# Kernel optimization log

Hardware: AMD Instinct MI355X
Metric: run time of the kernel (lower is better)

The kernel has to match this reference:

```python
import jax, jax.numpy as jnp
import numpy as np
import math

EMBED_DIM = 512
NUM_HEADS = 8
B, T = 1, 4096

def setup_inputs() -> dict:
    key = jax.random.key(0)
    ks = jax.random.split(key, 12)
    D = EMBED_DIM
    s = 1.0 / math.sqrt(D)
    inp = {
        "x": jax.random.normal(ks[0], (B, T, D), dtype=jnp.float32),
        "ln1_scale": jnp.ones((D,), jnp.float32),
        "ln1_bias": jnp.zeros((D,), jnp.float32),
        "Wq": jax.random.normal(ks[1], (D, D), jnp.float32) * s,
        "bq": jnp.zeros((D,), jnp.float32),
        "Wk": jax.random.normal(ks[2], (D, D), jnp.float32) * s,
        "bk": jnp.zeros((D,), jnp.float32),
        "Wv": jax.random.normal(ks[3], (D, D), jnp.float32) * s,
        "bv": jnp.zeros((D,), jnp.float32),
        "Wo": jax.random.normal(ks[4], (D, D), jnp.float32) * s,
        "bo": jnp.zeros((D,), jnp.float32),
        "ln2_scale": jnp.ones((D,), jnp.float32),
        "ln2_bias": jnp.zeros((D,), jnp.float32),
        "W1": jax.random.normal(ks[5], (D, 4 * D), jnp.float32) * s,
        "b1": jnp.zeros((4 * D,), jnp.float32),
        "W2": jax.random.normal(ks[6], (4 * D, D), jnp.float32) * (1.0 / math.sqrt(4 * D)),
        "b2": jnp.zeros((D,), jnp.float32),
    }
    return inp

def _layernorm(x, scale, bias, eps=1e-6):
    mu = jnp.mean(x, axis=-1, keepdims=True)
    var = jnp.mean(jnp.square(x - mu), axis=-1, keepdims=True)
    return (x - mu) * jax.lax.rsqrt(var + eps) * scale + bias

def reference(x, ln1_scale, ln1_bias, Wq, bq, Wk, bk, Wv, bv, Wo, bo,
              ln2_scale, ln2_bias, W1, b1, W2, b2):
    Bb, Tt, D = x.shape
    H = NUM_HEADS
    hd = D // H
    residual = x
    h = _layernorm(x, ln1_scale, ln1_bias)
    q = (h @ Wq + bq).reshape(Bb, Tt, H, hd).transpose(0, 2, 1, 3)
    k = (h @ Wk + bk).reshape(Bb, Tt, H, hd).transpose(0, 2, 1, 3)
    v = (h @ Wv + bv).reshape(Bb, Tt, H, hd).transpose(0, 2, 1, 3)
    # [B,H,T,T] scores (naive attention as in the original module)
    scores = jnp.einsum('bhqd,bhkd->bhqk', q, k) / math.sqrt(hd)
    probs = jax.nn.softmax(scores, axis=-1)
    out = jnp.einsum('bhqk,bhkd->bhqd', probs, v).transpose(0, 2, 1, 3).reshape(Bb, Tt, D)
    h = out @ Wo + bo  # dropout deterministic -> identity
    x = h + residual
    residual = x
    h = _layernorm(x, ln2_scale, ln2_bias)
    h = jax.nn.gelu(h @ W1 + b1, approximate=True)
    h = h @ W2 + b2
    return h + residual
```

## Files before the change

### kernel.cpp

```cpp
#include <hip/hip_runtime.h>
#include <hip/hip_bf16.h>
#include <stdint.h>

typedef __bf16 bf16;
typedef __bf16 bf16x4 __attribute__((ext_vector_type(4)));
typedef __bf16 bf16x8 __attribute__((ext_vector_type(8)));
typedef float  f32x4  __attribute__((ext_vector_type(4)));
typedef float  f32x16 __attribute__((ext_vector_type(16)));

#define MFMA16(A_, B_, C_) __builtin_amdgcn_mfma_f32_16x16x32_bf16((A_), (B_), (C_), 0, 0, 0)
#define MFMA32(A_, B_, C_) __builtin_amdgcn_mfma_f32_32x32x16_bf16((A_), (B_), (C_), 0, 0, 0)

#define QSCALE 0.1803368801111137f

__device__ __forceinline__ void gload_lds16(const void* g, void* l) {
  __builtin_amdgcn_global_load_lds(
      (const __attribute__((address_space(1))) unsigned int*)g,
      (__attribute__((address_space(3))) unsigned int*)l, 16, 0, 0);
}

__device__ __forceinline__ unsigned pk2(float lo, float hi_) {
  union { bf16 h[2]; unsigned u; } t;
  t.h[0] = (bf16)lo; t.h[1] = (bf16)hi_;
  return t.u;
}

__global__ __launch_bounds__(256) void prep(const float* __restrict__ Wq,
                                            const float* __restrict__ Wk,
                                            const float* __restrict__ Wv,
                                            const float* __restrict__ Wo,
                                            const float* __restrict__ W1,
                                            const float* __restrict__ W2,
                                            const float* __restrict__ bq,
                                            const float* __restrict__ bk,
                                            const float* __restrict__ bv,
                                            bf16* __restrict__ wqkvT, bf16* __restrict__ woT,
                                            bf16* __restrict__ w1T, bf16* __restrict__ w2T,
                                            float* __restrict__ bqkv) {
  const int b = blockIdx.x;
  if (b >= 768) {
    int i = (b - 768) * 256 + threadIdx.x;
    if (i < 1536)
      bqkv[i] = (i < 512) ? bq[i] * QSCALE : (i < 1024 ? bk[i - 512] : bv[i - 1024]);
    return;
  }
  const float* in; bf16* outp; int K, N, t; float sc = 1.f;
  if (b < 64)       { in = Wq; outp = wqkvT;              K = 512;  N = 512;  t = b;       sc = QSCALE; }
  else if (b < 128) { in = Wk; outp = wqkvT + 512 * 512;  K = 512;  N = 512;  t = b - 64;  }
  else if (b < 192) { in = Wv; outp = wqkvT + 1024 * 512; K = 512;  N = 512;  t = b - 128; }
  else if (b < 256) { in = Wo; outp = woT;                K = 512;  N = 512;  t = b - 192; }
  else if (b < 512) { in = W1; outp = w1T;                K = 512;  N = 2048; t = b - 256; }
  else              { in = W2; outp = w2T;                K = 2048; N = 512;  t = b - 512; }
  const int tx = K >> 6;
  const int k0 = (t % tx) * 64, n0 = (t / tx) * 64;
  __shared__ bf16 tile[64][72];
  const int tid = threadIdx.x;
#pragma unroll
  for (int s = 0; s < 16; ++s) {
    int j = tid + s * 256;
    int r = j >> 6, c = j & 63;
    tile[r][c] = (bf16)(in[(size_t)(k0 + r) * N + n0 + c] * sc);
  }
  __syncthreads();
#pragma unroll
  for (int s = 0; s < 16; ++s) {
    int j = tid + s * 256;
    int n = j >> 6, k = j & 63;
    outp[(size_t)(n0 + n) * K + k0 + k] = tile[k][n];
  }
}

__global__ __launch_bounds__(256) void ln_k(const float* __restrict__ x,
                                            const float* __restrict__ sc,
                                            const float* __restrict__ bi,
                                            bf16* __restrict__ out) {
  const int w = threadIdx.x >> 6, l = threadIdx.x & 63;
  const int row = blockIdx.x * 4 + w;
  const float4* xp = (const float4*)(x + (size_t)row * 512 + l * 8);
  float4 v0 = xp[0], v1 = xp[1];
  float xv[8] = {v0.x, v0.y, v0.z, v0.w, v1.x, v1.y, v1.z, v1.w};
  float s = 0.f, q = 0.f;
#pragma unroll
  for (int j = 0; j < 8; ++j) { s += xv[j]; q += xv[j] * xv[j]; }
#pragma unroll
  for (int m = 1; m < 64; m <<= 1) { s += __shfl_xor(s, m); q += __shfl_xor(q, m); }
  const float mean = s * (1.f / 512.f);
  const float var = q * (1.f / 512.f) - mean * mean;
  const float rstd = rsqrtf(var + 1e-6f);
  const float4* scp = (const float4*)(sc + l * 8);
  const float4* bip = (const float4*)(bi + l * 8);
  float4 s0 = scp[0], s1 = scp[1], b0 = bip[0], b1 = bip[1];
  float sv[8] = {s0.x, s0.y, s0.z, s0.w, s1.x, s1.y, s1.z, s1.w};
  float bv[8] = {b0.x, b0.y, b0.z, b0.w, b1.x, b1.y, b1.z, b1.w};
  bf16x8 ov;
#pragma unroll
  for (int j = 0; j < 8; ++j) ov[j] = (bf16)((xv[j] - mean) * rstd * sv[j] + bv[j]);
  *(bf16x8*)(out + (size_t)row * 512 + l * 8) = ov;
}

__global__ __launch_bounds__(256) void ln2_comb(const float* __restrict__ p0,
                                                const float* __restrict__ p1,
                                                const float* __restrict__ x,
                                                const float* __restrict__ bo,
                                                const float* __restrict__ sc,
                                                const float* __restrict__ bi,
                                                float* __restrict__ x2,
                                                bf16* __restrict__ h2) {
  const int w = threadIdx.x >> 6, l = threadIdx.x & 63;
  const int row = blockIdx.x * 4 + w;
  const size_t base = (size_t)row * 512 + l * 8;
  float xv[8];
#pragma unroll
  for (int j = 0; j < 2; ++j) {
    float4 a = *(const float4*)(p0 + base + j * 4);
    float4 b = *(const float4*)(p1 + base + j * 4);
    float4 c = *(const float4*)(x + base + j * 4);
    float4 d = *(const float4*)(bo + l * 8 + j * 4);
    xv[j * 4 + 0] = a.x + b.x + c.x + d.x;
    xv[j * 4 + 1] = a.y + b.y + c.y + d.y;
    xv[j * 4 + 2] = a.z + b.z + c.z + d.z;
    xv[j * 4 + 3] = a.w + b.w + c.w + d.w;
  }
  *(float4*)(x2 + base) = make_float4(xv[0], xv[1], xv[2], xv[3]);
  *(float4*)(x2 + base + 4) = make_float4(xv[4], xv[5], xv[6], xv[7]);
  float s = 0.f, q = 0.f;
#pragma unroll
  for (int j = 0; j < 8; ++j) { s += xv[j]; q += xv[j] * xv[j]; }
#pragma unroll
  for (int m = 1; m < 64; m <<= 1) { s += __shfl_xor(s, m); q += __shfl_xor(q, m); }
  const float mean = s * (1.f / 512.f);
  const float var = q * (1.f / 512.f) - mean * mean;
  const float rstd = rsqrtf(var + 1e-6f);
  const float4* scp = (const float4*)(sc + l * 8);
  const float4* bip = (const float4*)(bi + l * 8);
  float4 s0 = scp[0], s1 = scp[1], b0 = bip[0], b1 = bip[1];
  float sv[8] = {s0.x, s0.y, s0.z, s0.w, s1.x, s1.y, s1.z, s1.w};
  float bv[8] = {b0.x, b0.y, b0.z, b0.w, b1.x, b1.y, b1.z, b1.w};
  bf16x8 ov;
#pragma unroll
  for (int j = 0; j < 8; ++j) ov[j] = (bf16)((xv[j] - mean) * rstd * sv[j] + bv[j]);
  *(bf16x8*)(h2 + base) = ov;
}

__global__ __launch_bounds__(256) void final_comb(const float* __restrict__ parts, int nsplit,
                                                  const float* __restrict__ b2,
                                                  const float* __restrict__ x2,
                                                  float* __restrict__ outp) {
  const int i4 = blockIdx.x * 256 + threadIdx.x;
  const size_t off = (size_t)i4 * 4;
  float4 acc = *(const float4*)(x2 + off);
  float4 bb = *(const float4*)(b2 + (off & 511));
  acc.x += bb.x; acc.y += bb.y; acc.z += bb.z; acc.w += bb.w;
  for (int z = 0; z < nsplit; ++z) {
    float4 p = *(const float4*)(parts + (size_t)z * 4096 * 512 + off);
    acc.x += p.x; acc.y += p.y; acc.z += p.z; acc.w += p.w;
  }
  *(float4*)(outp + off) = acc;
}

template <int EPI>
__global__ __launch_bounds__(256) void gemm_bt(const bf16* __restrict__ A,
                                               const bf16* __restrict__ Bt,
                                               const float* __restrict__ bias,
                                               const float* __restrict__ res,
                                               void* __restrict__ outp,
                                               int M, int N, int K) {
  __shared__ bf16 a_lds[128 * 64];
  __shared__ bf16 b_lds[128 * 64];
  const int m0 = blockIdx.x * 128, n0 = blockIdx.y * 128;
  const int tid = threadIdx.x, l = tid & 63, w = tid >> 6;
  const int wm = w >> 1, wn = w & 1;
  const int lc = l & 15, g = l >> 4;
  const int srow = l >> 3;
  const int cs = (l & 7) ^ srow;

  f32x4 acc[4][4] = {};
  const int kiters = K >> 6;
  for (int kt = 0; kt < kiters; ++kt) {
    const int k0 = kt << 6;
#pragma unroll
    for (int r = 0; r < 4; ++r) {
      const int rg = r * 32 + w * 8;
      gload_lds16(A + (size_t)(m0 + rg + srow) * K + k0 + cs * 8,
                  (char*)a_lds + rg * 128);
      gload_lds16(Bt + (size_t)(n0 + rg + srow) * K + k0 + cs * 8,
                  (char*)b_lds + rg * 128);
    }
    __syncthreads();
#pragma unroll
    for (int kk = 0; kk < 2; ++kk) {
      bf16x8 af[4], bfr[4];
#pragma unroll
      for (int i = 0; i < 4; ++i) {
        const int sw = ((kk * 4 + g) ^ (lc & 7)) * 8;
        af[i]  = *(const bf16x8*)(a_lds + (wm * 64 + i * 16 + lc) * 64 + sw);
        bfr[i] = *(const bf16x8*)(b_lds + (wn * 64 + i * 16 + lc) * 64 + sw);
      }
#pragma unroll
      for (int mi = 0; mi < 4; ++mi)
#pragma unroll
        for (int ni = 0; ni < 4; ++ni)
          acc[mi][ni] = MFMA16(af[mi], bfr[ni], acc[mi][ni]);
    }
    __syncthreads();
  }

#pragma unroll
  for (int mi = 0; mi < 4; ++mi)
#pragma unroll
    for (int ni = 0; ni < 4; ++ni) {
      const int col = n0 + wn * 64 + ni * 16 + lc;
      const float bb = bias[col];
#pragma unroll
      for (int i = 0; i < 4; ++i) {
        const int row = m0 + wm * 64 + mi * 16 + g * 4 + i;
        float v = acc[mi][ni][i] + bb;
        if constexpr (EPI == 0) {
          ((bf16*)outp)[(size_t)row * N + col] = (bf16)v;
        } else if constexpr (EPI == 1) {
          ((float*)outp)[(size_t)row * N + col] = v + res[(size_t)row * N + col];
        } else {
          float t = -2.3022077697f * (v + 0.044715f * v * v * v);
          float gl = v / (1.f + exp2f(t));
          ((bf16*)outp)[(size_t)row * N + col] = (bf16)gl;
        }
      }
    }
}

__global__ __launch_bounds__(256) void gemm_skp(const bf16* __restrict__ A,
                                                const bf16* __restrict__ Bt,
                                                float* __restrict__ parts,
                                                int M, int N, int Kstride, int Kc) {
  __shared__ bf16 a_lds[128 * 64];
  __shared__ bf16 b_lds[128 * 64];
  const int m0 = blockIdx.x * 128, n0 = blockIdx.y * 128, kz = blockIdx.z;
  A += (size_t)kz * Kc;
  Bt += (size_t)kz * Kc;
  float* outp = parts + (size_t)kz * M * N;
  const int tid = threadIdx.x, l = tid & 63, w = tid >> 6;
  const int wm = w >> 1, wn = w & 1;
  const int lc = l & 15, g = l >> 4;
  const int srow = l >> 3;
  const int cs = (l & 7) ^ srow;

  f32x4 acc[4][4] = {};
  const int kiters = Kc >> 6;
  for (int kt = 0; kt < kiters; ++kt) {
    const int k0 = kt << 6;
#pragma unroll
    for (int r = 0; r < 4; ++r) {
      const int rg = r * 32 + w * 8;
      gload_lds16(A + (size_t)(m0 + rg + srow) * Kstride + k0 + cs * 8,
                  (char*)a_lds + rg * 128);
      gload_lds16(Bt + (size_t)(n0 + rg + srow) * Kstride + k0 + cs * 8,
                  (char*)b_lds + rg * 128);
    }
    __syncthreads();
#pragma unroll
    for (int kk = 0; kk < 2; ++kk) {
      bf16x8 af[4], bfr[4];
#pragma unroll
      for (int i = 0; i < 4; ++i) {
        const int sw = ((kk * 4 + g) ^ (lc & 7)) * 8;
        af[i]  = *(const bf16x8*)(a_lds + (wm * 64 + i * 16 + lc) * 64 + sw);
        bfr[i] = *(const bf16x8*)(b_lds + (wn * 64 + i * 16 + lc) * 64 + sw);
      }
#pragma unroll
      for (int mi = 0; mi < 4; ++mi)
#pragma unroll
        for (int ni = 0; ni < 4; ++ni)
          acc[mi][ni] = MFMA16(af[mi], bfr[ni], acc[mi][ni]);
    }
    __syncthreads();
  }

#pragma unroll
  for (int mi = 0; mi < 4; ++mi)
#pragma unroll
    for (int ni = 0; ni < 4; ++ni) {
      const int col = n0 + wn * 64 + ni * 16 + lc;
#pragma unroll
      for (int i = 0; i < 4; ++i) {
        const int row = m0 + wm * 64 + mi * 16 + g * 4 + i;
        outp[(size_t)row * N + col] = acc[mi][ni][i];
      }
    }
}

__global__ __launch_bounds__(256) void vtrans(const bf16* __restrict__ qkv,
                                              bf16* __restrict__ vt) {
  __shared__ bf16 tile[64][72];
  const int t0 = blockIdx.x * 64;
  const int head = blockIdx.y;
  const int tid = threadIdx.x;
#pragma unroll
  for (int s = 0; s < 16; ++s) {
    int j = tid + s * 256;
    int t = j >> 6, c = j & 63;
    tile[t][c] = qkv[(size_t)(t0 + t) * 1536 + 1024 + head * 64 + c];
  }
  __syncthreads();
#pragma unroll
  for (int s = 0; s < 16; ++s) {
    int j = tid + s * 256;
    int d = j >> 6, t = j & 63;
    vt[(size_t)head * 64 * 4096 + (size_t)d * 4096 + t0 + t] = tile[t][d];
  }
}

__global__ __launch_bounds__(256, 4) void attn_k(const bf16* __restrict__ qkv,
                                                 const bf16* __restrict__ vt,
                                                 bf16* __restrict__ opart,
                                                 float* __restrict__ lpart) {
  const int bid = blockIdx.x;
  const int head = bid & 7;
  const int qt = (bid >> 3) & 63;
  const int ks = bid >> 9;
  const int w = threadIdx.x >> 6, l = threadIdx.x & 63;
  const int hi = l >> 5, l5 = l & 31;
  const int pair = w >> 1, wq = w & 1;

  __shared__ char smem[32768];
  bf16* kt_l = (bf16*)(smem + pair * 8192);
  bf16* vt_l = (bf16*)(smem + 16384 + pair * 8192);

  const bf16* kg = qkv + 512 + head * 64;
  const bf16* vg = vt + (size_t)head * 64 * 4096;

  const int qrow0 = qt * 64 + wq * 32;
  const bf16* qb = qkv + (size_t)(qrow0 + l5) * 1536 + head * 64;
  bf16x8 qf[4];
#pragma unroll
  for (int cc = 0; cc < 4; ++cc) qf[cc] = *(const bf16x8*)(qb + cc * 16 + hi * 8);

  const int kstart = ks * 2048 + pair * 1024;
  const int srow = l >> 3;
  const int cs_k = (l & 7) ^ srow;
  const int cs_v = (l & 3) ^ ((l >> 3) & 3);

#pragma unroll
  for (int j = 0; j < 2; ++j) {
    const int rrk = wq * 16 + j * 8;
    gload_lds16(kg + (size_t)(kstart + rrk + srow) * 1536 + cs_k * 8,
                (char*)kt_l + rrk * 128);
    const int rgv = wq * 32 + j * 16;
    gload_lds16(vg + (size_t)(rgv + (l >> 2)) * 4096 + kstart + cs_v * 8,
                (char*)vt_l + rgv * 64);
  }
  __syncthreads();

  f32x16 o0 = {}, o1 = {};
  float psum = 0.f;
  const int swl = l5 & 7, swv = (l5 >> 1) & 3;

  for (int kt = 0; kt < 32; ++kt) {
    const int cur = kt & 1;
    if (kt < 31) {
      const int kv0 = kstart + (kt + 1) * 32;
#pragma unroll
      for (int j = 0; j < 2; ++j) {
        const int rrk = wq * 16 + j * 8;
        gload_lds16(kg + (size_t)(kv0 + rrk + srow) * 1536 + cs_k * 8,
                    (char*)kt_l + (cur ^ 1) * 4096 + rrk * 128);
        const int rgv = wq * 32 + j * 16;
        gload_lds16(vg + (size_t)(rgv + (l >> 2)) * 4096 + kv0 + cs_v * 8,
                    (char*)vt_l + (cur ^ 1) * 4096 + rgv * 64);
      }
    }
    const bf16* kb = kt_l + cur * 2048;
    const bf16* vb = vt_l + cur * 2048;

    f32x16 s = {};
#pragma unroll
    for (int cc = 0; cc < 4; ++cc) {
      bf16x8 kf = *(const bf16x8*)(kb + l5 * 64 + (((cc * 2 + hi) ^ swl) * 8));
      s = MFMA32(kf, qf[cc], s);
    }

#pragma unroll
    for (int c = 0; c < 2; ++c) {
      float p[8];
#pragma unroll
      for (int j = 0; j < 8; ++j) {
        p[j] = exp2f(s[c * 8 + j]);
        psum += p[j];
      }
      unsigned X = pk2(p[0], p[1]), X2 = pk2(p[2], p[3]);
      unsigned Y = pk2(p[4], p[5]), Y2 = pk2(p[6], p[7]);
      asm volatile("v_permlane32_swap_b32 %0, %1" : "+v"(X), "+v"(Y));
      asm volatile("v_permlane32_swap_b32 %0, %1" : "+v"(X2), "+v"(Y2));
      union { unsigned wd[4]; bf16x8 v; } pa;
      pa.wd[0] = X; pa.wd[1] = X2; pa.wd[2] = Y; pa.wd[3] = Y2;
      const int sw = ((c * 2 + hi) ^ swv) * 8;
      bf16x8 vf0 = *(const bf16x8*)(vb + l5 * 32 + sw);
      bf16x8 vf1 = *(const bf16x8*)(vb + (32 + l5) * 32 + sw);
      o0 = MFMA32(vf0, pa.v, o0);
      o1 = MFMA32(vf1, pa.v, o1);
    }
    __syncthreads();
  }

  float* comb = (float*)smem;
  if (w >= 2) {
    float* cb = comb + ((w - 2) * 64 + l) * 33;
#pragma unroll
    for (int r = 0; r < 16; ++r) { cb[r] = o0[r]; cb[16 + r] = o1[r]; }
    cb[32] = psum;
  }
  __syncthreads();
  if (w < 2) {
    const float* cb = comb + (w * 64 + l) * 33;
#pragma unroll
    for (int r = 0; r < 16; ++r) { o0[r] += cb[r]; o1[r] += cb[16 + r]; }
    psum += cb[32];
    const float lsum = psum + __shfl_xor(psum, 32);
    bf16* ob = opart + (size_t)ks * 4096 * 512 + (size_t)(qrow0 + l5) * 512 + head * 64;
#pragma unroll
    for (int dt = 0; dt < 2; ++dt)
#pragma unroll
      for (int rg = 0; rg < 4; ++rg) {
        bf16x4 vv;
#pragma unroll
        for (int e = 0; e < 4; ++e) {
          const float ov = (dt == 0) ? o0[rg * 4 + e] : o1[rg * 4 + e];
          vv[e] = (bf16)ov;
        }
        *(bf16x4*)(ob + dt * 32 + rg * 8 + hi * 4) = vv;
      }
    if (hi == 0) lpart[(ks * 8 + head) * 4096 + qrow0 + l5] = lsum;
  }
}

__global__ __launch_bounds__(256) void attn_comb(const bf16* __restrict__ op,
                                                 const float* __restrict__ lp,
                                                 bf16* __restrict__ ob) {
  const int idx = blockIdx.x * 256 + threadIdx.x;
  const int t = idx >> 6, c8 = idx & 63;
  const int head = c8 >> 3;
  const size_t o = (size_t)t * 512 + c8 * 8;
  bf16x8 a = *(const bf16x8*)(op + o);
  bf16x8 b = *(const bf16x8*)(op + 2097152 + o);
  const float inv = 1.f / (lp[head * 4096 + t] + lp[32768 + head * 4096 + t]);
  bf16x8 r;
#pragma unroll
  for (int j = 0; j < 8; ++j) r[j] = (bf16)(((float)a[j] + (float)b[j]) * inv);
  *(bf16x8*)(ob + o) = r;
}

extern "C" void kernel_launch(void* const* d_in, const int* in_sizes, int n_in,
                              void* d_out, int out_size, void* d_ws, size_t ws_size,
                              hipStream_t stream) {
  const float* x    = (const float*)d_in[0];
  const float* ln1s = (const float*)d_in[1];
  const float* ln1b = (const float*)d_in[2];
  const float* Wq   = (const float*)d_in[3];
  const float* bq   = (const float*)d_in[4];
  const float* Wk   = (const float*)d_in[5];
  const float* bk   = (const float*)d_in[6];
  const float* Wv   = (const float*)d_in[7];
  const float* bv   = (const float*)d_in[8];
  const float* Wo   = (const float*)d_in[9];
  const float* bo   = (const float*)d_in[10];
  const float* ln2s = (const float*)d_in[11];
  const float* ln2b = (const float*)d_in[12];
  const float* W1   = (const float*)d_in[13];
  const float* b1   = (const float*)d_in[14];
  const float* W2   = (const float*)d_in[15];
  const float* b2   = (const float*)d_in[16];
  float* out = (float*)d_out;

  char* ws = (char*)d_ws;
  bf16*  wqkvT = (bf16*)(ws + 0);
  bf16*  woT   = (bf16*)(ws + 1572864);
  bf16*  w1T   = (bf16*)(ws + 2097152);
  bf16*  w2T   = (bf16*)(ws + 4194304);
  float* bqkv  = (float*)(ws + 6291456);
  float* lpart = (float*)(ws + 6297600);
  bf16*  opart = (bf16*)(ws + 6559744);
  float* x2    = (float*)(ws + 6559744);
  bf16*  h     = (bf16*)(ws + 14948352);
  bf16*  qkv   = (bf16*)(ws + 19142656);
  bf16*  vt    = (bf16*)(ws + 31725568);
  bf16*  attnb = h;
  bf16*  h2    = h;
  float* wop   = (float*)(ws + 19142656);
  bf16*  gbuf  = qkv;
  float* f2p   = (float*)(ws + 35919872);
  const size_t need4 = 35919872 + 4ull * 8388608;
  const size_t need2 = 35919872 + 2ull * 8388608;

  prep<<<774, 256, 0, stream>>>(Wq, Wk, Wv, Wo, W1, W2, bq, bk, bv,
                                wqkvT, woT, w1T, w2T, bqkv);

  ln_k<<<1024, 256, 0, stream>>>(x, ln1s, ln1b, h);
  gemm_bt<0><<<dim3(32, 12), 256, 0, stream>>>(h, wqkvT, bqkv, nullptr, qkv, 4096, 1536, 512);
  vtrans<<<dim3(64, 8), 256, 0, stream>>>(qkv, vt);
  attn_k<<<1024, 256, 0, stream>>>(qkv, vt, opart, lpart);
  attn_comb<<<1024, 256, 0, stream>>>(opart, lpart, attnb);
  gemm_skp<<<dim3(32, 4, 2), 256, 0, stream>>>(attnb, woT, wop, 4096, 512, 512, 256);
  ln2_comb<<<1024, 256, 0, stream>>>(wop, wop + 4096 * 512, x, bo, ln2s, ln2b, x2, h2);
  gemm_bt<2><<<dim3(32, 16), 256, 0, stream>>>(h2, w1T, b1, nullptr, gbuf, 4096, 2048, 512);
  if (ws_size >= need4) {
    gemm_skp<<<dim3(32, 4, 4), 256, 0, stream>>>(gbuf, w2T, f2p, 4096, 512, 2048, 512);
    final_comb<<<2048, 256, 0, stream>>>(f2p, 4, b2, x2, out);
  } else if (ws_size >= need2) {
    gemm_skp<<<dim3(32, 4, 2), 256, 0, stream>>>(gbuf, w2T, f2p, 4096, 512, 2048, 1024);
    final_comb<<<2048, 256, 0, stream>>>(f2p, 2, b2, x2, out);
  } else {
    gemm_bt<1><<<dim3(32, 4), 256, 0, stream>>>(gbuf, w2T, b2, x2, out, 4096, 512, 2048);
  }
}
```

Baseline: 161.9 us.

## Drop attention split-K combine, give each wave private K/V buffers, fast exp2

The attention kernel no longer splits the key range across two blocks. Each block now covers all 4096 keys, two wave pairs split the range internally, and the output is normalised in-kernel, so the separate combine kernel and its partial buffers are removed. Each wave gets its own double-buffered K/V LDS region (64KB per block), synchronised with s_waitcnt vmcnt instead of per-tile __syncthreads. It also raises priority around the MFMA section and switches exp2 to the hardware builtin, including in the GELU epilogue. The cost is a grid halved to 512 blocks, lower occupancy from launch bounds 2 and the larger LDS footprint, and each wave now loads K/V on its own, which adds load traffic.

```diff
diff --git a/kernel.cpp b/kernel.cpp
--- a/kernel.cpp
+++ b/kernel.cpp
@@ -23,6 +23,14 @@
   union { bf16 h[2]; unsigned u; } t;
   t.h[0] = (bf16)lo; t.h[1] = (bf16)hi_;
   return t.u;
+}
+
+__device__ __forceinline__ float fast_exp2(float x) {
+#if __has_builtin(__builtin_amdgcn_exp2f)
+  return __builtin_amdgcn_exp2f(x);
+#else
+  return exp2f(x);
+#endif
 }
 
 __global__ __launch_bounds__(256) void prep(const float* __restrict__ Wq,
@@ -221,7 +229,7 @@
           ((float*)outp)[(size_t)row * N + col] = v + res[(size_t)row * N + col];
         } else {
           float t = -2.3022077697f * (v + 0.044715f * v * v * v);
-          float gl = v / (1.f + exp2f(t));
+          float gl = v / (1.f + fast_exp2(t));
           ((bf16*)outp)[(size_t)row * N + col] = (bf16)gl;
         }
       }
@@ -309,21 +317,19 @@
   }
 }
 
-__global__ __launch_bounds__(256, 4) void attn_k(const bf16* __restrict__ qkv,
+__global__ __launch_bounds__(256, 2) void attn_k(const bf16* __restrict__ qkv,
                                                  const bf16* __restrict__ vt,
-                                                 bf16* __restrict__ opart,
-                                                 float* __restrict__ lpart) {
+                                                 bf16* __restrict__ out) {
   const int bid = blockIdx.x;
   const int head = bid & 7;
-  const int qt = (bid >> 3) & 63;
-  const int ks = bid >> 9;
+  const int qt = bid >> 3;
   const int w = threadIdx.x >> 6, l = threadIdx.x & 63;
   const int hi = l >> 5, l5 = l & 31;
   const int pair = w >> 1, wq = w & 1;
 
-  __shared__ char smem[32768];
-  bf16* kt_l = (bf16*)(smem + pair * 8192);
-  bf16* vt_l = (bf16*)(smem + 16384 + pair * 8192);
+  __shared__ __align__(16) char smem[65536];
+  char* kt_l = smem + w * 16384;
+  char* vt_l = kt_l + 8192;
 
   const bf16* kg = qkv + 512 + head * 64;
   const bf16* vg = vt + (size_t)head * 64 * 4096;
@@ -334,43 +340,42 @@
 #pragma unroll
   for (int cc = 0; cc < 4; ++cc) qf[cc] = *(const bf16x8*)(qb + cc * 16 + hi * 8);
 
-  const int kstart = ks * 2048 + pair * 1024;
+  const int kstart = pair * 2048;
   const int srow = l >> 3;
-  const int cs_k = (l & 7) ^ srow;
-  const int cs_v = (l & 3) ^ ((l >> 3) & 3);
-
-#pragma unroll
-  for (int j = 0; j < 2; ++j) {
-    const int rrk = wq * 16 + j * 8;
-    gload_lds16(kg + (size_t)(kstart + rrk + srow) * 1536 + cs_k * 8,
-                (char*)kt_l + rrk * 128);
-    const int rgv = wq * 32 + j * 16;
-    gload_lds16(vg + (size_t)(rgv + (l >> 2)) * 4096 + kstart + cs_v * 8,
-                (char*)vt_l + rgv * 64);
-  }
-  __syncthreads();
+  const int cl = (l & 7) ^ srow;
+  const bf16* kgl = kg + (size_t)(kstart + srow) * 1536 + cl * 8;
+  const bf16* vgl = vg + (size_t)((cl >> 2) * 32 + srow) * 4096 + kstart + (cl & 3) * 8;
+
+#define STAGE_A(T_, B_)                                                     \
+  do {                                                                      \
+    const int kv0_ = (T_) * 32;                                             \
+    _Pragma("unroll")                                                       \
+    for (int j_ = 0; j_ < 4; ++j_) {                                        \
+      gload_lds16(kgl + (size_t)(kv0_ + j_ * 8) * 1536,                     \
+                  kt_l + (B_) * 4096 + j_ * 1024);                          \
+      gload_lds16(vgl + (size_t)(j_ * 8) * 4096 + kv0_,                     \
+                  vt_l + (B_) * 4096 + j_ * 1024);                          \
+    }                                                                       \
+  } while (0)
+
+  STAGE_A(0, 0);
 
   f32x16 o0 = {}, o1 = {};
   float psum = 0.f;
-  const int swl = l5 & 7, swv = (l5 >> 1) & 3;
-
-  for (int kt = 0; kt < 32; ++kt) {
-    const int cur = kt & 1;
-    if (kt < 31) {
-      const int kv0 = kstart + (kt + 1) * 32;
-#pragma unroll
-      for (int j = 0; j < 2; ++j) {
-        const int rrk = wq * 16 + j * 8;
-        gload_lds16(kg + (size_t)(kv0 + rrk + srow) * 1536 + cs_k * 8,
-                    (char*)kt_l + (cur ^ 1) * 4096 + rrk * 128);
-        const int rgv = wq * 32 + j * 16;
-        gload_lds16(vg + (size_t)(rgv + (l >> 2)) * 4096 + kv0 + cs_v * 8,
-                    (char*)vt_l + (cur ^ 1) * 4096 + rgv * 64);
-      }
-    }
-    const bf16* kb = kt_l + cur * 2048;
-    const bf16* vb = vt_l + cur * 2048;
-
+  const int swl = l5 & 7;
+
+  for (int t = 0; t < 64; ++t) {
+    const int cur = t & 1;
+    if (t < 63) {
+      STAGE_A(t + 1, cur ^ 1);
+      asm volatile("s_waitcnt vmcnt(8)" ::: "memory");
+    } else {
+      asm volatile("s_waitcnt vmcnt(0)" ::: "memory");
+    }
+    const bf16* kb = (const bf16*)(kt_l + cur * 4096);
+    const bf16* vb = (const bf16*)(vt_l + cur * 4096);
+
+    __builtin_amdgcn_s_setprio(1);
     f32x16 s = {};
 #pragma unroll
     for (int cc = 0; cc < 4; ++cc) {
@@ -382,25 +387,24 @@
     for (int c = 0; c < 2; ++c) {
       float p[8];
 #pragma unroll
-      for (int j = 0; j < 8; ++j) {
-        p[j] = exp2f(s[c * 8 + j]);
-        psum += p[j];
-      }
+      for (int j = 0; j < 8; ++j) p[j] = fast_exp2(s[c * 8 + j]);
+      psum += ((p[0] + p[1]) + (p[2] + p[3])) + ((p[4] + p[5]) + (p[6] + p[7]));
       unsigned X = pk2(p[0], p[1]), X2 = pk2(p[2], p[3]);
       unsigned Y = pk2(p[4], p[5]), Y2 = pk2(p[6], p[7]);
       asm volatile("v_permlane32_swap_b32 %0, %1" : "+v"(X), "+v"(Y));
       asm volatile("v_permlane32_swap_b32 %0, %1" : "+v"(X2), "+v"(Y2));
       union { unsigned wd[4]; bf16x8 v; } pa;
       pa.wd[0] = X; pa.wd[1] = X2; pa.wd[2] = Y; pa.wd[3] = Y2;
-      const int sw = ((c * 2 + hi) ^ swv) * 8;
-      bf16x8 vf0 = *(const bf16x8*)(vb + l5 * 32 + sw);
-      bf16x8 vf1 = *(const bf16x8*)(vb + (32 + l5) * 32 + sw);
+      bf16x8 vf0 = *(const bf16x8*)(vb + l5 * 64 + (((c * 2 + hi) ^ swl) * 8));
+      bf16x8 vf1 = *(const bf16x8*)(vb + l5 * 64 + (((4 + c * 2 + hi) ^ swl) * 8));
       o0 = MFMA32(vf0, pa.v, o0);
       o1 = MFMA32(vf1, pa.v, o1);
     }
-    __syncthreads();
-  }
-
+    __builtin_amdgcn_s_setprio(0);
+  }
+#undef STAGE_A
+
+  __syncthreads();
   float* comb = (float*)smem;
   if (w >= 2) {
     float* cb = comb + ((w - 2) * 64 + l) * 33;
@@ -415,7 +419,8 @@
     for (int r = 0; r < 16; ++r) { o0[r] += cb[r]; o1[r] += cb[16 + r]; }
     psum += cb[32];
     const float lsum = psum + __shfl_xor(psum, 32);
-    bf16* ob = opart + (size_t)ks * 4096 * 512 + (size_t)(qrow0 + l5) * 512 + head * 64;
+    const float inv = 1.f / lsum;
+    bf16* ob = out + (size_t)(qrow0 + l5) * 512 + head * 64;
 #pragma unroll
     for (int dt = 0; dt < 2; ++dt)
 #pragma unroll
@@ -424,28 +429,11 @@
 #pragma unroll
         for (int e = 0; e < 4; ++e) {
           const float ov = (dt == 0) ? o0[rg * 4 + e] : o1[rg * 4 + e];
-          vv[e] = (bf16)ov;
+          vv[e] = (bf16)(ov * inv);
         }
         *(bf16x4*)(ob + dt * 32 + rg * 8 + hi * 4) = vv;
       }
-    if (hi == 0) lpart[(ks * 8 + head) * 4096 + qrow0 + l5] = lsum;
-  }
-}
-
-__global__ __launch_bounds__(256) void attn_comb(const bf16* __restrict__ op,
-                                                 const float* __restrict__ lp,
-                                                 bf16* __restrict__ ob) {
-  const int idx = blockIdx.x * 256 + threadIdx.x;
-  const int t = idx >> 6, c8 = idx & 63;
-  const int head = c8 >> 3;
-  const size_t o = (size_t)t * 512 + c8 * 8;
-  bf16x8 a = *(const bf16x8*)(op + o);
-  bf16x8 b = *(const bf16x8*)(op + 2097152 + o);
-  const float inv = 1.f / (lp[head * 4096 + t] + lp[32768 + head * 4096 + t]);
-  bf16x8 r;
-#pragma unroll
-  for (int j = 0; j < 8; ++j) r[j] = (bf16)(((float)a[j] + (float)b[j]) * inv);
-  *(bf16x8*)(ob + o) = r;
+  }
 }
 
 extern "C" void kernel_launch(void* const* d_in, const int* in_sizes, int n_in,
@@ -476,8 +464,6 @@
   bf16*  w1T   = (bf16*)(ws + 2097152);
   bf16*  w2T   = (bf16*)(ws + 4194304);
   float* bqkv  = (float*)(ws + 6291456);
-  float* lpart = (float*)(ws + 6297600);
-  bf16*  opart = (bf16*)(ws + 6559744);
   float* x2    = (float*)(ws + 6559744);
   bf16*  h     = (bf16*)(ws + 14948352);
   bf16*  qkv   = (bf16*)(ws + 19142656);
@@ -496,8 +482,7 @@
   ln_k<<<1024, 256, 0, stream>>>(x, ln1s, ln1b, h);
   gemm_bt<0><<<dim3(32, 12), 256, 0, stream>>>(h, wqkvT, bqkv, nullptr, qkv, 4096, 1536, 512);
   vtrans<<<dim3(64, 8), 256, 0, stream>>>(qkv, vt);
-  attn_k<<<1024, 256, 0, stream>>>(qkv, vt, opart, lpart);
-  attn_comb<<<1024, 256, 0, stream>>>(opart, lpart, attnb);
+  attn_k<<<512, 256, 0, stream>>>(qkv, vt, attnb);
   gemm_skp<<<dim3(32, 4, 2), 256, 0, stream>>>(attnb, woT, wop, 4096, 512, 512, 256);
   ln2_comb<<<1024, 256, 0, stream>>>(wop, wop + 4096 * 512, x, bo, ln2s, ln2b, x2, h2);
   gemm_bt<2><<<dim3(32, 16), 256, 0, stream>>>(h2, w1T, b1, nullptr, gbuf, 4096, 2048, 512);
```

Measured after the change: 161.5 us. About the same (-0.3%).

## Repack K/V per head and load attention operands directly from global memory

Applied to the files above, without the earlier changes.

The transpose kernel now also packs K into a contiguous per-head layout and stores V in 32-token tiles. The attention kernel then reads MFMA fragments straight from global/L2 instead of staging them through double-buffered LDS with per-tile barriers, and it raises wave priority around the MFMAs. It also switches exp2 to the hardware intrinsic in attention and GELU. This removes the LDS traffic and the barrier in the loop, at the cost of an extra K copy, more global-load latency exposed per iteration, and a larger workspace.

```diff
diff --git a/kernel.cpp b/kernel.cpp
--- a/kernel.cpp
+++ b/kernel.cpp
@@ -23,6 +23,14 @@
   union { bf16 h[2]; unsigned u; } t;
   t.h[0] = (bf16)lo; t.h[1] = (bf16)hi_;
   return t.u;
+}
+
+__device__ __forceinline__ float fast_exp2(float x) {
+#if __has_builtin(__builtin_amdgcn_exp2f)
+  return __builtin_amdgcn_exp2f(x);
+#else
+  return exp2f(x);
+#endif
 }
 
 __global__ __launch_bounds__(256) void prep(const float* __restrict__ Wq,
@@ -221,7 +229,7 @@
           ((float*)outp)[(size_t)row * N + col] = v + res[(size_t)row * N + col];
         } else {
           float t = -2.3022077697f * (v + 0.044715f * v * v * v);
-          float gl = v / (1.f + exp2f(t));
+          float gl = v / (1.f + fast_exp2(t));
           ((bf16*)outp)[(size_t)row * N + col] = (bf16)gl;
         }
       }
@@ -288,8 +296,9 @@
     }
 }
 
-__global__ __launch_bounds__(256) void vtrans(const bf16* __restrict__ qkv,
-                                              bf16* __restrict__ vt) {
+__global__ __launch_bounds__(256) void repack(const bf16* __restrict__ qkv,
+                                              bf16* __restrict__ k2,
+                                              bf16* __restrict__ v2) {
   __shared__ bf16 tile[64][72];
   const int t0 = blockIdx.x * 64;
   const int head = blockIdx.y;
@@ -297,6 +306,13 @@
 #pragma unroll
   for (int s = 0; s < 16; ++s) {
     int j = tid + s * 256;
+    int t = j >> 6, d = j & 63;
+    k2[(size_t)head * 262144 + (size_t)(t0 + t) * 64 + d] =
+        qkv[(size_t)(t0 + t) * 1536 + 512 + head * 64 + d];
+  }
+#pragma unroll
+  for (int s = 0; s < 16; ++s) {
+    int j = tid + s * 256;
     int t = j >> 6, c = j & 63;
     tile[t][c] = qkv[(size_t)(t0 + t) * 1536 + 1024 + head * 64 + c];
   }
@@ -305,12 +321,14 @@
   for (int s = 0; s < 16; ++s) {
     int j = tid + s * 256;
     int d = j >> 6, t = j & 63;
-    vt[(size_t)head * 64 * 4096 + (size_t)d * 4096 + t0 + t] = tile[t][d];
+    v2[(size_t)head * 262144 + (size_t)((t0 >> 5) + (t >> 5)) * 2048 + d * 32 + (t & 31)] =
+        tile[t][d];
   }
 }
 
 __global__ __launch_bounds__(256, 4) void attn_k(const bf16* __restrict__ qkv,
-                                                 const bf16* __restrict__ vt,
+                                                 const bf16* __restrict__ k2,
+                                                 const bf16* __restrict__ v2,
                                                  bf16* __restrict__ opart,
                                                  float* __restrict__ lpart) {
   const int bid = blockIdx.x;
@@ -321,12 +339,10 @@
   const int hi = l >> 5, l5 = l & 31;
   const int pair = w >> 1, wq = w & 1;
 
-  __shared__ char smem[32768];
-  bf16* kt_l = (bf16*)(smem + pair * 8192);
-  bf16* vt_l = (bf16*)(smem + 16384 + pair * 8192);
-
-  const bf16* kg = qkv + 512 + head * 64;
-  const bf16* vg = vt + (size_t)head * 64 * 4096;
+  __shared__ float comb[2 * 64 * 33];
+
+  const bf16* kg = k2 + (size_t)head * 262144;
+  const bf16* vg = v2 + (size_t)head * 262144;
 
   const int qrow0 = qt * 64 + wq * 32;
   const bf16* qb = qkv + (size_t)(qrow0 + l5) * 1536 + head * 64;
@@ -335,73 +351,48 @@
   for (int cc = 0; cc < 4; ++cc) qf[cc] = *(const bf16x8*)(qb + cc * 16 + hi * 8);
 
   const int kstart = ks * 2048 + pair * 1024;
-  const int srow = l >> 3;
-  const int cs_k = (l & 7) ^ srow;
-  const int cs_v = (l & 3) ^ ((l >> 3) & 3);
-
-#pragma unroll
-  for (int j = 0; j < 2; ++j) {
-    const int rrk = wq * 16 + j * 8;
-    gload_lds16(kg + (size_t)(kstart + rrk + srow) * 1536 + cs_k * 8,
-                (char*)kt_l + rrk * 128);
-    const int rgv = wq * 32 + j * 16;
-    gload_lds16(vg + (size_t)(rgv + (l >> 2)) * 4096 + kstart + cs_v * 8,
-                (char*)vt_l + rgv * 64);
-  }
-  __syncthreads();
 
   f32x16 o0 = {}, o1 = {};
   float psum = 0.f;
-  const int swl = l5 & 7, swv = (l5 >> 1) & 3;
-
-  for (int kt = 0; kt < 32; ++kt) {
-    const int cur = kt & 1;
-    if (kt < 31) {
-      const int kv0 = kstart + (kt + 1) * 32;
-#pragma unroll
-      for (int j = 0; j < 2; ++j) {
-        const int rrk = wq * 16 + j * 8;
-        gload_lds16(kg + (size_t)(kv0 + rrk + srow) * 1536 + cs_k * 8,
-                    (char*)kt_l + (cur ^ 1) * 4096 + rrk * 128);
-        const int rgv = wq * 32 + j * 16;
-        gload_lds16(vg + (size_t)(rgv + (l >> 2)) * 4096 + kv0 + cs_v * 8,
-                    (char*)vt_l + (cur ^ 1) * 4096 + rgv * 64);
-      }
-    }
-    const bf16* kb = kt_l + cur * 2048;
-    const bf16* vb = vt_l + cur * 2048;
-
+
+#pragma unroll 2
+  for (int t = 0; t < 32; ++t) {
+    const int kv0 = kstart + t * 32;
+    const bf16* kb = kg + (size_t)kv0 * 64 + l5 * 64 + hi * 8;
+    const bf16* vp = vg + (size_t)(kv0 >> 5) * 2048;
+    bf16x8 kf0 = *(const bf16x8*)(kb);
+    bf16x8 kf1 = *(const bf16x8*)(kb + 16);
+    bf16x8 kf2 = *(const bf16x8*)(kb + 32);
+    bf16x8 kf3 = *(const bf16x8*)(kb + 48);
+    __builtin_amdgcn_s_setprio(1);
     f32x16 s = {};
-#pragma unroll
-    for (int cc = 0; cc < 4; ++cc) {
-      bf16x8 kf = *(const bf16x8*)(kb + l5 * 64 + (((cc * 2 + hi) ^ swl) * 8));
-      s = MFMA32(kf, qf[cc], s);
-    }
+    s = MFMA32(kf0, qf[0], s);
+    s = MFMA32(kf1, qf[1], s);
+    s = MFMA32(kf2, qf[2], s);
+    s = MFMA32(kf3, qf[3], s);
+    __builtin_amdgcn_s_setprio(0);
 
 #pragma unroll
     for (int c = 0; c < 2; ++c) {
+      bf16x8 vf0 = *(const bf16x8*)(vp + l5 * 32 + c * 16 + hi * 8);
+      bf16x8 vf1 = *(const bf16x8*)(vp + (32 + l5) * 32 + c * 16 + hi * 8);
       float p[8];
 #pragma unroll
-      for (int j = 0; j < 8; ++j) {
-        p[j] = exp2f(s[c * 8 + j]);
-        psum += p[j];
-      }
+      for (int j = 0; j < 8; ++j) p[j] = fast_exp2(s[c * 8 + j]);
+      psum += ((p[0] + p[1]) + (p[2] + p[3])) + ((p[4] + p[5]) + (p[6] + p[7]));
       unsigned X = pk2(p[0], p[1]), X2 = pk2(p[2], p[3]);
       unsigned Y = pk2(p[4], p[5]), Y2 = pk2(p[6], p[7]);
       asm volatile("v_permlane32_swap_b32 %0, %1" : "+v"(X), "+v"(Y));
       asm volatile("v_permlane32_swap_b32 %0, %1" : "+v"(X2), "+v"(Y2));
       union { unsigned wd[4]; bf16x8 v; } pa;
       pa.wd[0] = X; pa.wd[1] = X2; pa.wd[2] = Y; pa.wd[3] = Y2;
-      const int sw = ((c * 2 + hi) ^ swv) * 8;
-      bf16x8 vf0 = *(const bf16x8*)(vb + l5 * 32 + sw);
-      bf16x8 vf1 = *(const bf16x8*)(vb + (32 + l5) * 32 + sw);
+      __builtin_amdgcn_s_setprio(1);
       o0 = MFMA32(vf0, pa.v, o0);
       o1 = MFMA32(vf1, pa.v, o1);
-    }
-    __syncthreads();
-  }
-
-  float* comb = (float*)smem;
+      __builtin_amdgcn_s_setprio(0);
+    }
+  }
+
   if (w >= 2) {
     float* cb = comb + ((w - 2) * 64 + l) * 33;
 #pragma unroll
@@ -481,22 +472,23 @@
   float* x2    = (float*)(ws + 6559744);
   bf16*  h     = (bf16*)(ws + 14948352);
   bf16*  qkv   = (bf16*)(ws + 19142656);
-  bf16*  vt    = (bf16*)(ws + 31725568);
+  bf16*  k2    = (bf16*)(ws + 31725568);
+  bf16*  v2    = (bf16*)(ws + 35919872);
   bf16*  attnb = h;
   bf16*  h2    = h;
   float* wop   = (float*)(ws + 19142656);
   bf16*  gbuf  = qkv;
-  float* f2p   = (float*)(ws + 35919872);
-  const size_t need4 = 35919872 + 4ull * 8388608;
-  const size_t need2 = 35919872 + 2ull * 8388608;
+  float* f2p   = (float*)(ws + 40114176);
+  const size_t need4 = 40114176 + 4ull * 8388608;
+  const size_t need2 = 40114176 + 2ull * 8388608;
 
   prep<<<774, 256, 0, stream>>>(Wq, Wk, Wv, Wo, W1, W2, bq, bk, bv,
                                 wqkvT, woT, w1T, w2T, bqkv);
 
   ln_k<<<1024, 256, 0, stream>>>(x, ln1s, ln1b, h);
   gemm_bt<0><<<dim3(32, 12), 256, 0, stream>>>(h, wqkvT, bqkv, nullptr, qkv, 4096, 1536, 512);
-  vtrans<<<dim3(64, 8), 256, 0, stream>>>(qkv, vt);
-  attn_k<<<1024, 256, 0, stream>>>(qkv, vt, opart, lpart);
+  repack<<<dim3(64, 8), 256, 0, stream>>>(qkv, k2, v2);
+  attn_k<<<1024, 256, 0, stream>>>(qkv, k2, v2, opart, lpart);
   attn_comb<<<1024, 256, 0, stream>>>(opart, lpart, attnb);
   gemm_skp<<<dim3(32, 4, 2), 256, 0, stream>>>(attnb, woT, wop, 4096, 512, 512, 256);
   ln2_comb<<<1024, 256, 0, stream>>>(wop, wop + 4096 * 512, x, bo, ln2s, ln2b, x2, h2);
```

Result: slower. 188.3 us (+16.3%).
